# Kernel tuning notes

Measured on AMD Instinct MI355X. Metric: run time of the kernel, lower is better.

Reference implementation:

```python
import jax, jax.numpy as jnp
import numpy as np

DT = 0.02
TMAX = 3.0
NUM_T = 151  # arange(0, Tmax+dt, dt) -> indices 0..150, 150*dt == Tmax == nonspike
THRESH = 1.0
TIMELINE = jnp.arange(NUM_T, dtype=jnp.float32) * DT          # [T]
TIMELINE_REV = jnp.flip(TIMELINE) + 0.1                        # [T]


def linear_spike_fwd(ti, W):
    """ti: [B, Fin] spike times; W: [Fout, Fin] -> out: [B, Fout] spike times."""
    # ramp: relu(t - ti)  -> [B, Fin, T]
    tmp = jax.nn.relu(TIMELINE[None, None, :] - ti[:, :, None])
    # membrane voltage: mem[b,j,t] = sum_i W[j,i] * tmp[b,i,t]  -> [B, Fout, T]
    mem = jnp.einsum('bit,ji->bjt', tmp, W)
    binary = (mem >= THRESH).astype(jnp.float32)
    binary = binary.at[:, :, -1].set(1.0)  # force spike at last timestep
    # reversed-timeline weighting makes argmax pick the FIRST spike index
    idx = jnp.argmax(binary * TIMELINE_REV, axis=2)
    return idx.astype(jnp.float32) * DT


def setup_inputs() -> dict:
    key = jax.random.key(0)
    k1, k2, k3 = jax.random.split(key, 3)
    B, F0, F1, F2 = 64, 1876, 1024, 10
    ti = jax.random.uniform(k1, (B, F0), dtype=jnp.float32)  # spike times in [0,1)
    W1 = 0.002 + 0.002 * jax.random.normal(k2, (F1, F0), dtype=jnp.float32)
    W2 = 0.001 + 0.001 * jax.random.normal(k3, (F2, F1), dtype=jnp.float32)
    return {"ti": ti, "W1": W1, "W2": W2}


def reference(ti, W1, W2):
    h1 = linear_spike_fwd(ti, W1)
    h2 = linear_spike_fwd(h1, W2)
    return h2
```

## Files before the change

kernel.cpp:

```cpp
#include <hip/hip_runtime.h>
#include <stdint.h>

namespace {

constexpr int   B_    = 64;
constexpr int   F0_   = 1876;
constexpr int   F1_   = 1024;
constexpr int   F2_   = 10;
constexpr int   NT_   = 151;
constexpr float DT_   = 0.02f;
constexpr int   NSTR_ = 1920;
constexpr int   CHUNK_= 480;
constexpr int   NGRP_ = 60;
constexpr int   NB1_  = 51;
constexpr float SCL_  = 67108864.0f;
constexpr float ISCL_ = 1.0f / 67108864.0f;

constexpr size_t OFF_W1T  = 0;
constexpr size_t OFF_PAIR = 7864320;
constexpr size_t OFF_IDX1 = OFF_PAIR + 983040;

__global__ __launch_bounds__(256) void k_w1t(const float* __restrict__ W1,
                                             float* __restrict__ W1T) {
  __shared__ float tile[64][65];
  const int i0 = blockIdx.x * 64;
  const int j0 = blockIdx.y * 64;
  const int t  = threadIdx.x;
  const int c  = t & 63, r4 = t >> 6;
  for (int jj = r4; jj < 64; jj += 4) {
    int i = i0 + c;
    float v = (i < F0_) ? W1[(size_t)(j0 + jj) * F0_ + i] : 0.0f;
    tile[c][jj] = v;
  }
  __syncthreads();
  for (int ii = r4; ii < 64; ii += 4) {
    int i = i0 + ii;
    W1T[(size_t)i * F1_ + j0 + c] = tile[ii][c];
  }
}

__global__ __launch_bounds__(256) void k_sort1(const float* __restrict__ ti,
                                               uint2* __restrict__ sPair) {
  __shared__ uint32_t hist[256][NB1_];
  __shared__ uint32_t bstart[NB1_ + 1];
  const int b = blockIdx.x, t = threadIdx.x;
  for (int k = 0; k < NB1_; ++k) hist[t][k] = 0;
  __syncthreads();

  const float* tib = ti + (size_t)b * F0_;
  const int n0 = t * 8;
  const int n1 = (n0 + 8 < F0_) ? n0 + 8 : F0_;
  for (int n = n0; n < n1; ++n) {
    int k = (int)ceilf(tib[n] * 50.0f);
    k = k < 0 ? 0 : (k > 50 ? 50 : k);
    hist[t][k]++;
  }
  __syncthreads();

  if (t < NB1_) {
    uint32_t run = 0;
    for (int c = 0; c < 256; ++c) { uint32_t x = hist[c][t]; hist[c][t] = run; run += x; }
    bstart[t + 1] = run;
  }
  __syncthreads();
  if (t == 0) {
    bstart[0] = 0;
    uint32_t acc = 0;
    for (int k = 0; k < NB1_; ++k) { uint32_t c = bstart[k + 1]; bstart[k + 1] = acc + c; acc += c; }
  }
  __syncthreads();

  uint2* out = sPair + (size_t)b * NSTR_;
  for (int n = n0; n < n1; ++n) {
    float v = tib[n];
    int k = (int)ceilf(v * 50.0f);
    k = k < 0 ? 0 : (k > 50 ? 50 : k);
    uint32_t pos = bstart[k] + hist[t][k]++;
    out[pos] = make_uint2(((uint32_t)n << 12) | (uint32_t)k, __float_as_uint(v));
  }
  for (int s = t; s < NSTR_ - F0_; s += 256)
    out[F0_ + s] = make_uint2(((uint32_t)F0_ << 12) | 80u, __float_as_uint(1.6f));
}

__global__ __launch_bounds__(256) void k_main1(const uint2* __restrict__ sPair,
                                               const float* __restrict__ W1T,
                                               uint8_t* __restrict__ idx1) {
  __shared__ int  binAi[NB1_][64];
  __shared__ int  binCi[NB1_][64];
  __shared__ int  cand[4][64];
  const int blk  = blockIdx.x;
  const int b    = blk >> 4;
  const int jp   = blk & 15;
  const int tid  = threadIdx.x;
  const int lane = tid & 63;
  const int wv   = __builtin_amdgcn_readfirstlane(tid >> 6);

  for (int s = tid; s < NB1_ * 64; s += 256) {
    (&binAi[0][0])[s] = 0;
    (&binCi[0][0])[s] = 0;
  }
  __syncthreads();

  const uint2* __restrict__ spw = sPair + (size_t)b * NSTR_ + wv * CHUNK_;
  const char*  __restrict__ wb  = (const char*)W1T;
  const uint32_t col4 = (uint32_t)(jp * 64 + lane) * 4u;

  float SA = 0.f, SC = 0.f, SAp = 0.f, SCp = 0.f;
  uint32_t kcur;

  uint2 Pb[3][8];
  float W[3][8];

#define RDP(buf, g) {                                                         \
  _Pragma("unroll") for (int e = 0; e < 8; ++e) Pb[buf][e] = spw[(g) * 8 + e]; }

#define ISSW(buf) {                                                           \
  _Pragma("unroll") for (int e = 0; e < 8; ++e) {                             \
    W[buf][e] = *(const float*)(wb + (Pb[buf][e].x & ~4095u) + col4); } }

#define DUMP() { if (kcur < (uint32_t)NB1_) {                                 \
    atomicAdd(&binAi[kcur][lane], __float2int_rn((SA - SAp) * SCL_));         \
    atomicAdd(&binCi[kcur][lane], __float2int_rn((SC - SCp) * SCL_)); }       \
  SAp = SA; SCp = SC; }

#define PROC(buf) {                                                           \
  uint32_t kend = Pb[buf][7].x & 4095u;                                       \
  if (kend == kcur) {                \
    _Pragma("unroll") for (int e = 0; e < 8; ++e) {                           \
      float w = W[buf][e];                                                    \
      SA += w; SC = fmaf(w, __uint_as_float(Pb[buf][e].y), SC); }             \
  } else {                                                                    \
    _Pragma("unroll") for (int e = 0; e < 8; ++e) {                           \
      uint32_t kb = Pb[buf][e].x & 4095u;                                     \
      if (kb != kcur) { DUMP(); kcur = kb; }                                  \
      float w = W[buf][e];                                                    \
      SA += w; SC = fmaf(w, __uint_as_float(Pb[buf][e].y), SC); }             \
  } }

  RDP(0, 0); RDP(1, 1);
  ISSW(0);
  RDP(2, 2);
  ISSW(1);
  kcur = Pb[0][0].x & 4095u;

#pragma unroll 1
  for (int k = 0; k < NGRP_ - 3; k += 3) {
    ISSW(2); PROC(0); RDP(0, k + 3);
    ISSW(0); PROC(1); RDP(1, k + 4);
    ISSW(1); PROC(2); RDP(2, k + 5);
  }
  ISSW(2);
  PROC(0);
  PROC(1);
  PROC(2);
  DUMP();

#undef PROC
#undef DUMP
#undef ISSW
#undef RDP

  __syncthreads();

  {
    float SA2 = 0.f, SC2 = 0.f;
    int cnd = 151;
    const int t0 = wv * 38;
    const int t1 = (wv == 3) ? NT_ : t0 + 38;
    for (int t = 0; t < t1; ++t) {
      if (t < NB1_) {
        SA2 += (float)binAi[t][lane] * ISCL_;
        SC2 += (float)binCi[t][lane] * ISCL_;
      }
      if (t >= t0 && cnd == 151) {
        float m = (float)t * DT_ * SA2 - SC2;
        if (m >= 1.0f) cnd = t;
      }
    }
    cand[wv][lane] = cnd;
  }
  __syncthreads();
  if (tid < 64) {
    int id = min(min(cand[0][lane], cand[1][lane]),
                 min(cand[2][lane], cand[3][lane]));
    id = min(id, NT_ - 1);
    idx1[((size_t)b << 10) + (jp << 6) + lane] = (uint8_t)id;
  }
}

__global__ __launch_bounds__(256) void k_main2(const uint8_t* __restrict__ idx1,
                                               const float* __restrict__ W2,
                                               float* __restrict__ out) {
  __shared__ float wrow[F1_];
  __shared__ float tirow[F1_];
  __shared__ float part[4][3][64];
  const int blk = blockIdx.x;
  const int b   = blk / 10;
  const int j   = blk - b * 10;
  const int tid = threadIdx.x;
  const int lane = tid & 63, wvv = tid >> 6;

  const float*   w = W2  + (size_t)j * F1_;
  const uint8_t* h = idx1 + (size_t)b * F1_;
  for (int s = tid; s < F1_; s += 256) {
    wrow[s]  = w[s];
    tirow[s] = (float)h[s] * DT_;
  }
  __syncthreads();

  const float tl0 = (float)lane * DT_;
  const float tl1 = (float)(lane + 64) * DT_;
  const float tl2 = (float)(lane + 128) * DT_;
  float m0 = 0.f, m1 = 0.f, m2 = 0.f;
  const int i0 = wvv * 256;
#pragma unroll 4
  for (int i = i0; i < i0 + 256; ++i) {
    float tiv = tirow[i], ww = wrow[i];
    m0 = fmaf(ww, fmaxf(tl0 - tiv, 0.f), m0);
    m1 = fmaf(ww, fmaxf(tl1 - tiv, 0.f), m1);
    m2 = fmaf(ww, fmaxf(tl2 - tiv, 0.f), m2);
  }
  part[wvv][0][lane] = m0;
  part[wvv][1][lane] = m1;
  part[wvv][2][lane] = m2;
  __syncthreads();

  if (wvv == 0) {
    m0 = part[0][0][lane] + part[1][0][lane] + part[2][0][lane] + part[3][0][lane];
    m1 = part[0][1][lane] + part[1][1][lane] + part[2][1][lane] + part[3][1][lane];
    m2 = part[0][2][lane] + part[1][2][lane] + part[2][2][lane] + part[3][2][lane];
    unsigned long long b0 = __ballot(m0 >= 1.0f);
    unsigned long long b1 = __ballot(m1 >= 1.0f);
    unsigned long long b2 = __ballot(m2 >= 1.0f);
    b2 &= (1ull << 23) - 1;
    b2 |= (1ull << 22);
    int tres;
    if (b0)      tres = __ffsll((long long)b0) - 1;
    else if (b1) tres = 64 + __ffsll((long long)b1) - 1;
    else         tres = 128 + __ffsll((long long)b2) - 1;
    if (lane == 0) out[(size_t)b * F2_ + j] = (float)tres * DT_;
  }
}

}

extern "C" void kernel_launch(void* const* d_in, const int* in_sizes, int n_in,
                              void* d_out, int out_size, void* d_ws, size_t ws_size,
                              hipStream_t stream) {
  const float* ti = (const float*)d_in[0];
  const float* W1 = (const float*)d_in[1];
  const float* W2 = (const float*)d_in[2];
  float* out = (float*)d_out;

  char* ws = (char*)d_ws;
  float*   W1T  = (float*)(ws + OFF_W1T);
  uint2*   sPr  = (uint2*)(ws + OFF_PAIR);
  uint8_t* idx1 = (uint8_t*)(ws + OFF_IDX1);

  hipLaunchKernelGGL(k_w1t,   dim3(30, 16), dim3(256), 0, stream, W1, W1T);
  hipLaunchKernelGGL(k_sort1, dim3(64),     dim3(256), 0, stream, ti, sPr);
  hipLaunchKernelGGL(k_main1, dim3(1024),   dim3(256), 0, stream, sPr, W1T, idx1);
  hipLaunchKernelGGL(k_main2, dim3(640),    dim3(256), 0, stream, idx1, W2, out);
}
```

Baseline: 77.38 us.

## Process two output columns per lane with 8-wave blocks in spike accumulation

The main layer-1 kernel now has each lane load a float2 from the transposed weights and accumulate two output neurons, so each sorted (index, time) pair is reused across twice as many columns. Blocks grow to 512 threads (8 waves), each wave scanning a shorter 256-entry chunk of a sorted list padded to 2048, with a 4-deep load pipeline. The transpose kernel stops writing rows past the padding row, which shrinks the workspace. In exchange, register pressure and LDS use per block go up, and there are half as many blocks, which may reduce latency hiding.

```diff
diff --git a/kernel.cpp b/kernel.cpp
--- a/kernel.cpp
+++ b/kernel.cpp
@@ -9,16 +9,16 @@
 constexpr int   F2_   = 10;
 constexpr int   NT_   = 151;
 constexpr float DT_   = 0.02f;
-constexpr int   NSTR_ = 1920;
-constexpr int   CHUNK_= 480;
-constexpr int   NGRP_ = 60;
+constexpr int   NSTR_ = 2048;
+constexpr int   CHUNK_= 256;
+constexpr int   NGRP_ = 32;
 constexpr int   NB1_  = 51;
 constexpr float SCL_  = 67108864.0f;
 constexpr float ISCL_ = 1.0f / 67108864.0f;
 
 constexpr size_t OFF_W1T  = 0;
-constexpr size_t OFF_PAIR = 7864320;
-constexpr size_t OFF_IDX1 = OFF_PAIR + 983040;
+constexpr size_t OFF_PAIR = 7688192;
+constexpr size_t OFF_IDX1 = OFF_PAIR + 1048576;
 
 __global__ __launch_bounds__(256) void k_w1t(const float* __restrict__ W1,
                                              float* __restrict__ W1T) {
@@ -35,7 +35,7 @@
   __syncthreads();
   for (int ii = r4; ii < 64; ii += 4) {
     int i = i0 + ii;
-    W1T[(size_t)i * F1_ + j0 + c] = tile[ii][c];
+    if (i <= F0_) W1T[(size_t)i * F1_ + j0 + c] = tile[ii][c];
   }
 }
 
@@ -82,79 +82,88 @@
     out[F0_ + s] = make_uint2(((uint32_t)F0_ << 12) | 80u, __float_as_uint(1.6f));
 }
 
-__global__ __launch_bounds__(256) void k_main1(const uint2* __restrict__ sPair,
+__global__ __launch_bounds__(512) void k_main1(const uint2* __restrict__ sPair,
                                                const float* __restrict__ W1T,
                                                uint8_t* __restrict__ idx1) {
-  __shared__ int  binAi[NB1_][64];
-  __shared__ int  binCi[NB1_][64];
-  __shared__ int  cand[4][64];
+  __shared__ int binAi[NB1_][128];
+  __shared__ int binCi[NB1_][128];
+  __shared__ int cand[4][128];
   const int blk  = blockIdx.x;
-  const int b    = blk >> 4;
-  const int jp   = blk & 15;
+  const int b    = blk >> 3;
+  const int jp   = blk & 7;
   const int tid  = threadIdx.x;
   const int lane = tid & 63;
   const int wv   = __builtin_amdgcn_readfirstlane(tid >> 6);
 
-  for (int s = tid; s < NB1_ * 64; s += 256) {
-    (&binAi[0][0])[s] = 0;
-    (&binCi[0][0])[s] = 0;
+  {
+    int4* p = (int4*)(&binAi[0][0]);
+    const int ntot = (NB1_ * 128 * 2) / 4;
+    for (int s = tid; s < ntot; s += 512) p[s] = make_int4(0, 0, 0, 0);
   }
   __syncthreads();
 
   const uint2* __restrict__ spw = sPair + (size_t)b * NSTR_ + wv * CHUNK_;
   const char*  __restrict__ wb  = (const char*)W1T;
-  const uint32_t col4 = (uint32_t)(jp * 64 + lane) * 4u;
-
-  float SA = 0.f, SC = 0.f, SAp = 0.f, SCp = 0.f;
+  const uint32_t col8 = (uint32_t)(jp * 512 + lane * 8);
+
+  float SA0 = 0.f, SC0 = 0.f, SA1 = 0.f, SC1 = 0.f;
+  float SA0p = 0.f, SC0p = 0.f, SA1p = 0.f, SC1p = 0.f;
   uint32_t kcur;
 
-  uint2 Pb[3][8];
-  float W[3][8];
+  uint2  Pb[4][8];
+  float2 W[4][8];
 
 #define RDP(buf, g) {                                                         \
   _Pragma("unroll") for (int e = 0; e < 8; ++e) Pb[buf][e] = spw[(g) * 8 + e]; }
 
 #define ISSW(buf) {                                                           \
   _Pragma("unroll") for (int e = 0; e < 8; ++e) {                             \
-    W[buf][e] = *(const float*)(wb + (Pb[buf][e].x & ~4095u) + col4); } }
+    W[buf][e] = *(const float2*)(wb + (Pb[buf][e].x & ~4095u) + col8); } }
 
 #define DUMP() { if (kcur < (uint32_t)NB1_) {                                 \
-    atomicAdd(&binAi[kcur][lane], __float2int_rn((SA - SAp) * SCL_));         \
-    atomicAdd(&binCi[kcur][lane], __float2int_rn((SC - SCp) * SCL_)); }       \
-  SAp = SA; SCp = SC; }
+    atomicAdd(&binAi[kcur][2 * lane],     __float2int_rn((SA0 - SA0p) * SCL_)); \
+    atomicAdd(&binCi[kcur][2 * lane],     __float2int_rn((SC0 - SC0p) * SCL_)); \
+    atomicAdd(&binAi[kcur][2 * lane + 1], __float2int_rn((SA1 - SA1p) * SCL_)); \
+    atomicAdd(&binCi[kcur][2 * lane + 1], __float2int_rn((SC1 - SC1p) * SCL_)); } \
+  SA0p = SA0; SC0p = SC0; SA1p = SA1; SC1p = SC1; }
 
 #define PROC(buf) {                                                           \
   uint32_t kend = Pb[buf][7].x & 4095u;                                       \
-  if (kend == kcur) {                \
+  if (kend == kcur) {            \
     _Pragma("unroll") for (int e = 0; e < 8; ++e) {                           \
-      float w = W[buf][e];                                                    \
-      SA += w; SC = fmaf(w, __uint_as_float(Pb[buf][e].y), SC); }             \
+      float2 w = W[buf][e];                                                   \
+      float tiv = __uint_as_float(Pb[buf][e].y);                              \
+      SA0 += w.x; SC0 = fmaf(w.x, tiv, SC0);                                  \
+      SA1 += w.y; SC1 = fmaf(w.y, tiv, SC1); }                                \
   } else {                                                                    \
     _Pragma("unroll") for (int e = 0; e < 8; ++e) {                           \
       uint32_t kb = Pb[buf][e].x & 4095u;                                     \
       if (kb != kcur) { DUMP(); kcur = kb; }                                  \
-      float w = W[buf][e];                                                    \
-      SA += w; SC = fmaf(w, __uint_as_float(Pb[buf][e].y), SC); }             \
+      float2 w = W[buf][e];                                                   \
+      float tiv = __uint_as_float(Pb[buf][e].y);                              \
+      SA0 += w.x; SC0 = fmaf(w.x, tiv, SC0);                                  \
+      SA1 += w.y; SC1 = fmaf(w.y, tiv, SC1); }                                \
   } }
 
-  RDP(0, 0); RDP(1, 1);
-  ISSW(0);
-  RDP(2, 2);
-  ISSW(1);
+#define HALF(b0, b1, b2, b3, g)                                               \
+  ISSW(b2); PROC(b0); RDP(b0, (g) + 4);                                       \
+  ISSW(b3); PROC(b1); RDP(b1, (g) + 5);
+
+  RDP(0, 0); RDP(1, 1); RDP(2, 2); RDP(3, 3);
+  ISSW(0); ISSW(1);
   kcur = Pb[0][0].x & 4095u;
 
 #pragma unroll 1
-  for (int k = 0; k < NGRP_ - 3; k += 3) {
-    ISSW(2); PROC(0); RDP(0, k + 3);
-    ISSW(0); PROC(1); RDP(1, k + 4);
-    ISSW(1); PROC(2); RDP(2, k + 5);
-  }
-  ISSW(2);
-  PROC(0);
-  PROC(1);
-  PROC(2);
+  for (int g = 0; g <= NGRP_ - 8; g += 4) {
+    HALF(0, 1, 2, 3, g);
+    HALF(2, 3, 0, 1, g + 2);
+  }
+  ISSW(2); PROC(0);
+  ISSW(3); PROC(1);
+  PROC(2); PROC(3);
   DUMP();
 
+#undef HALF
 #undef PROC
 #undef DUMP
 #undef ISSW
@@ -163,28 +172,30 @@
   __syncthreads();
 
   {
+    const int jh = wv & 1, tq = wv >> 1;
+    const int col = jh * 64 + lane;
     float SA2 = 0.f, SC2 = 0.f;
     int cnd = 151;
-    const int t0 = wv * 38;
-    const int t1 = (wv == 3) ? NT_ : t0 + 38;
+    const int t0 = tq * 38;
+    const int t1 = (tq == 3) ? NT_ : t0 + 38;
     for (int t = 0; t < t1; ++t) {
       if (t < NB1_) {
-        SA2 += (float)binAi[t][lane] * ISCL_;
-        SC2 += (float)binCi[t][lane] * ISCL_;
+        SA2 += (float)binAi[t][col] * ISCL_;
+        SC2 += (float)binCi[t][col] * ISCL_;
       }
       if (t >= t0 && cnd == 151) {
         float m = (float)t * DT_ * SA2 - SC2;
         if (m >= 1.0f) cnd = t;
       }
     }
-    cand[wv][lane] = cnd;
-  }
-  __syncthreads();
-  if (tid < 64) {
-    int id = min(min(cand[0][lane], cand[1][lane]),
-                 min(cand[2][lane], cand[3][lane]));
+    cand[tq][col] = cnd;
+  }
+  __syncthreads();
+  if (tid < 128) {
+    int id = min(min(cand[0][tid], cand[1][tid]),
+                 min(cand[2][tid], cand[3][tid]));
     id = min(id, NT_ - 1);
-    idx1[((size_t)b << 10) + (jp << 6) + lane] = (uint8_t)id;
+    idx1[((size_t)b << 10) + (jp << 7) + tid] = (uint8_t)id;
   }
 }
 
@@ -259,6 +270,6 @@
 
   hipLaunchKernelGGL(k_w1t,   dim3(30, 16), dim3(256), 0, stream, W1, W1T);
   hipLaunchKernelGGL(k_sort1, dim3(64),     dim3(256), 0, stream, ti, sPr);
-  hipLaunchKernelGGL(k_main1, dim3(1024),   dim3(256), 0, stream, sPr, W1T, idx1);
+  hipLaunchKernelGGL(k_main1, dim3(512),    dim3(512), 0, stream, sPr, W1T, idx1);
   hipLaunchKernelGGL(k_main2, dim3(640),    dim3(256), 0, stream, idx1, W2, out);
 }
```

After: 80.05 us. +3.5%, slower.
